# Kernel tuning notes

Hardware: AMD Instinct MI355X
Metric: run time of the kernel (lower is better)

## Reference

```python
import jax, jax.numpy as jnp
import numpy as np

EMBED_DIM = 1024
N_TOKENS = 8192


def setup_inputs() -> dict:
    key = jax.random.key(0)
    k1, k2, k3 = jax.random.split(key, 3)
    inputs = jax.random.normal(k1, (N_TOKENS, EMBED_DIM), dtype=jnp.float32)
    rotation_params = jax.random.normal(k2, (EMBED_DIM, EMBED_DIM), dtype=jnp.float32)
    entangle_params = jax.random.normal(k3, (EMBED_DIM, EMBED_DIM), dtype=jnp.float32)
    return {"inputs": inputs, "rotation_params": rotation_params, "entangle_params": entangle_params}


def reference(inputs, rotation_params, entangle_params):
    # query/key projections from externally supplied params
    embed_dim = inputs.shape[-1]
    wq = rotation_params.reshape(embed_dim, -1)
    wk = entangle_params.reshape(embed_dim, -1)
    query = inputs @ wq          # [N, d]
    key = inputs @ wk            # [N, d]
    scale = 1.0 / jnp.sqrt(jnp.float32(embed_dim))
    scores = jax.nn.softmax(jnp.einsum('nd,md->nm', query, key) * scale, axis=-1)  # [N, N]
    context = scores @ inputs    # attend over raw inputs (V = inputs)
    return context
```

## Files before the change

kernel.cpp:

```cpp
#include <hip/hip_runtime.h>
#include <hip/hip_bf16.h>


typedef _Float16 f16x8 __attribute__((ext_vector_type(8)));
typedef _Float16 f16x4 __attribute__((ext_vector_type(4)));
typedef float    f32x4 __attribute__((ext_vector_type(4)));

#define TM 128
#define TN 128

__device__ __forceinline__ void g2lds16(const _Float16* g, _Float16* l) {
    __builtin_amdgcn_global_load_lds(
        (__attribute__((address_space(1))) unsigned int*)(g),
        (__attribute__((address_space(3))) unsigned int*)(l),
        16, 0, 0);
}


__global__ void prep_x(const float* __restrict__ src,
                       _Float16* __restrict__ hi, _Float16* __restrict__ lo,
                       _Float16* __restrict__ xt, int R, int C) {
    __shared__ float tile[32][33];
    int c0 = blockIdx.x * 32, r0 = blockIdx.y * 32;
    int tx = threadIdx.x, ty = threadIdx.y;
#pragma unroll
    for (int k = 0; k < 4; ++k) {
        int r = ty + 8 * k;
        size_t idx = (size_t)(r0 + r) * C + c0 + tx;
        float v = src[idx];
        tile[r][tx] = v;
        _Float16 h = (_Float16)v;
        hi[idx] = h;
        lo[idx] = (_Float16)(v - (float)h);
    }
    __syncthreads();
#pragma unroll
    for (int k = 0; k < 4; ++k) {
        float v = tile[tx][ty + 8 * k];
        xt[(size_t)(c0 + ty + 8 * k) * R + r0 + tx] = (_Float16)v;
    }
}

__global__ void transpose_split(const float* __restrict__ src,
                                _Float16* __restrict__ dhi,
                                _Float16* __restrict__ dlo,
                                int R, int C) {
    __shared__ float tile[32][33];
    int c0 = blockIdx.x * 32, r0 = blockIdx.y * 32;
    int tx = threadIdx.x, ty = threadIdx.y;
#pragma unroll
    for (int k = 0; k < 4; ++k)
        tile[ty + 8 * k][tx] = src[(size_t)(r0 + ty + 8 * k) * C + c0 + tx];
    __syncthreads();
#pragma unroll
    for (int k = 0; k < 4; ++k) {
        float v = tile[tx][ty + 8 * k];
        _Float16 h = (_Float16)v;
        size_t idx = (size_t)(c0 + ty + 8 * k) * R + r0 + tx;
        dhi[idx] = h;
        dlo[idx] = (_Float16)(v - (float)h);
    }
}

__global__ __launch_bounds__(256) void add_rows(const float* __restrict__ a,
                                                const float* __restrict__ b,
                                                float* __restrict__ out, long n4) {
    long i = (long)blockIdx.x * blockDim.x + threadIdx.x;
    long stride = (long)gridDim.x * blockDim.x;
    for (; i < n4; i += stride) {
        float4 x = ((const float4*)a)[i];
        float4 y = ((const float4*)b)[i];
        x.x += y.x; x.y += y.y; x.z += y.z; x.w += y.w;
        ((float4*)out)[i] = x;
    }
}

template <int TERMS, int SPLIT_OUT, int SWAP, int BKH>
__global__ __launch_bounds__(256, 4) void gemm_bt(
    const _Float16* __restrict__ Ahi, const _Float16* __restrict__ Alo,
    const _Float16* __restrict__ Bhi, const _Float16* __restrict__ Blo,
    float* __restrict__ C, _Float16* __restrict__ Chi, _Float16* __restrict__ Clo,
    long lda, long ldb, long ldc, int K, long zA, long zB, long zC) {
    constexpr int NBUF = (TERMS == 3) ? 4 : 2;
    __shared__ __align__(16) _Float16 s[NBUF * 128 * BKH];

    const long z = blockIdx.z;
    Ahi += z * zA;
    Bhi += z * zB;
    if constexpr (TERMS == 3) { Alo += z * zA; Blo += z * zB; }
    if constexpr (SPLIT_OUT) { Chi += z * zC; Clo += z * zC; }
    else C += z * zC;

    const int t = threadIdx.x;
    const int wave = t >> 6;
    const int lane = t & 63;
    const int lm = lane & 15;
    const int lq = lane >> 4;
    const int wr = wave >> 1;
    const int wc = wave & 1;

    const long rowBase = (long)(SWAP ? blockIdx.x : blockIdx.y) * TM;
    const long colBase = (long)(SWAP ? blockIdx.y : blockIdx.x) * TN;

    const _Float16* src;
    long myLd, gRow0;
    int ldsBaseH;
    if constexpr (TERMS == 3) {
        const _Float16* a = (wave & 1) ? Alo : Ahi;
        const _Float16* b = (wave & 1) ? Blo : Bhi;
        src = (wave & 2) ? b : a;
        myLd = (wave & 2) ? ldb : lda;
        gRow0 = (wave & 2) ? colBase : rowBase;
        ldsBaseH = wave * (128 * BKH);
    } else {
        src = (wave & 2) ? Bhi : Ahi;
        myLd = (wave & 2) ? ldb : lda;
        gRow0 = ((wave & 2) ? colBase : rowBase) + (wave & 1) * 64;
        ldsBaseH = (wave >> 1) * (128 * BKH) + (wave & 1) * (64 * BKH);
    }
    constexpr int LPR = BKH / 8;
    constexpr int RPI = 64 / LPR;
    constexpr int NISS = (TERMS == 3 ? 128 : 64) / RPI;
    const int lr = lane / LPR;
    const int slot = lane % LPR;
    const int swzW = (BKH == 32) ? ((lr >> 1) & 3) : (lr & 7);
    const _Float16* rp = src + (gRow0 + lr) * myLd + (slot ^ swzW) * 8;
    _Float16* ldsW = &s[ldsBaseH];

    const _Float16* sAh = s;
    const _Float16* sBh = s + (TERMS == 3 ? 2 : 1) * 128 * BKH;
    const _Float16* sAl = s + 128 * BKH;
    const _Float16* sBl = s + 3 * 128 * BKH;

    const int swzR = (BKH == 32) ? ((lm >> 1) & 3) : (lm & 7);

    f32x4 acc[4][4];
#pragma unroll
    for (int r = 0; r < 4; ++r)
#pragma unroll
        for (int c = 0; c < 4; ++c)
#pragma unroll
            for (int i = 0; i < 4; ++i) acc[r][c][i] = 0.0f;

    for (int k0 = 0; k0 < K; k0 += BKH) {
        __syncthreads();
#pragma unroll
        for (int j = 0; j < NISS; ++j)
            g2lds16(rp + (long)(j * RPI) * myLd + k0, ldsW + j * 512);
        __syncthreads();

#pragma unroll
        for (int kk = 0; kk < BKH; kk += 32) {
            const int gb = kk >> 3;
            f16x8 ah[4], bh[4], al[4], bl[4];
#pragma unroll
            for (int r = 0; r < 4; ++r) {
                int ra = (wr * 64 + r * 16 + lm) * BKH + ((gb + lq) ^ swzR) * 8;
                int rb = (wc * 64 + r * 16 + lm) * BKH + ((gb + lq) ^ swzR) * 8;
                ah[r] = *(const f16x8*)&sAh[ra];
                bh[r] = *(const f16x8*)&sBh[rb];
                if constexpr (TERMS == 3) {
                    al[r] = *(const f16x8*)&sAl[ra];
                    bl[r] = *(const f16x8*)&sBl[rb];
                }
            }
#pragma unroll
            for (int r = 0; r < 4; ++r)
#pragma unroll
                for (int c = 0; c < 4; ++c) {
                    acc[r][c] = __builtin_amdgcn_mfma_f32_16x16x32_f16(
                        ah[r], bh[c], acc[r][c], 0, 0, 0);
                    if constexpr (TERMS == 3) {
                        acc[r][c] = __builtin_amdgcn_mfma_f32_16x16x32_f16(
                            ah[r], bl[c], acc[r][c], 0, 0, 0);
                        acc[r][c] = __builtin_amdgcn_mfma_f32_16x16x32_f16(
                            al[r], bh[c], acc[r][c], 0, 0, 0);
                    }
                }
        }
    }

#pragma unroll
    for (int r = 0; r < 4; ++r)
#pragma unroll
        for (int c = 0; c < 4; ++c)
#pragma unroll
            for (int i = 0; i < 4; ++i) {
                long row = rowBase + wr * 64 + r * 16 + lq * 4 + i;
                long col = colBase + wc * 64 + c * 16 + lm;
                if constexpr (SPLIT_OUT) {
                    float v = acc[r][c][i];
                    _Float16 h = (_Float16)v;
                    Chi[row * ldc + col] = h;
                    Clo[row * ldc + col] = (_Float16)(v - (float)h);
                } else {
                    C[row * ldc + col] = acc[r][c][i];
                }
            }
}

__global__ __launch_bounds__(256) void softmax_rows(const float* __restrict__ S,
                                                    _Float16* __restrict__ P,
                                                    long ldp, int N) {
    const int row = blockIdx.x;
    const int t = threadIdx.x;
    const float4* rowp = (const float4*)(S + (size_t)row * N);
    float4 v[8];
    float mx = -3.4e38f;
#pragma unroll
    for (int g = 0; g < 4; ++g) {
        v[2 * g]     = rowp[2 * t + 512 * g];
        v[2 * g + 1] = rowp[2 * t + 512 * g + 1];
    }
#pragma unroll
    for (int i = 0; i < 8; ++i)
        mx = fmaxf(mx, fmaxf(fmaxf(v[i].x, v[i].y), fmaxf(v[i].z, v[i].w)));
    __shared__ float red[8];
#pragma unroll
    for (int off = 32; off >= 1; off >>= 1) mx = fmaxf(mx, __shfl_xor(mx, off));
    if ((t & 63) == 0) red[t >> 6] = mx;
    __syncthreads();
    mx = fmaxf(fmaxf(red[0], red[1]), fmaxf(red[2], red[3]));

    float sum = 0.0f;
#pragma unroll
    for (int i = 0; i < 8; ++i) {
        v[i].x = __expf((v[i].x - mx) * 0.03125f);
        v[i].y = __expf((v[i].y - mx) * 0.03125f);
        v[i].z = __expf((v[i].z - mx) * 0.03125f);
        v[i].w = __expf((v[i].w - mx) * 0.03125f);
        sum += (v[i].x + v[i].y) + (v[i].z + v[i].w);
    }
#pragma unroll
    for (int off = 32; off >= 1; off >>= 1) sum += __shfl_xor(sum, off);
    if ((t & 63) == 0) red[4 + (t >> 6)] = sum;
    __syncthreads();
    float inv = 1.0f / (red[4] + red[5] + red[6] + red[7]);

    f16x8* prow = (f16x8*)(P + (size_t)row * ldp);
#pragma unroll
    for (int g = 0; g < 4; ++g) {
        float4 a = v[2 * g], b = v[2 * g + 1];
        f16x8 o;
        o[0] = (_Float16)(a.x * inv); o[1] = (_Float16)(a.y * inv);
        o[2] = (_Float16)(a.z * inv); o[3] = (_Float16)(a.w * inv);
        o[4] = (_Float16)(b.x * inv); o[5] = (_Float16)(b.y * inv);
        o[6] = (_Float16)(b.z * inv); o[7] = (_Float16)(b.w * inv);
        prow[t + 256 * g] = o;
    }
}

extern "C" void kernel_launch(void* const* d_in, const int* in_sizes, int n_in,
                              void* d_out, int out_size, void* d_ws, size_t ws_size,
                              hipStream_t stream) {
    const float* X  = (const float*)d_in[0];
    const float* Wq = (const float*)d_in[1];
    const float* Wk = (const float*)d_in[2];
    float* out = (float*)d_out;

    const long Nt = 8192, D = 1024;
    char* ws = (char*)d_ws;
    const size_t MB = 1024ull * 1024ull;

    _Float16* XT  = (_Float16*)(ws + 0);
    _Float16* Qhi = (_Float16*)(ws + 16 * MB);
    _Float16* Qlo = (_Float16*)(ws + 32 * MB);
    _Float16* Khi = (_Float16*)(ws + 48 * MB);
    _Float16* Klo = (_Float16*)(ws + 64 * MB);
    _Float16* Xhi   = (_Float16*)(ws + 80 * MB);
    _Float16* Xlo   = (_Float16*)(ws + 96 * MB);
    _Float16* WqThi = (_Float16*)(ws + 112 * MB);
    _Float16* WqTlo = (_Float16*)(ws + 114 * MB);
    _Float16* WkThi = (_Float16*)(ws + 116 * MB);
    _Float16* WkTlo = (_Float16*)(ws + 118 * MB);
    float* PK0 = (float*)(ws + 16 * MB);

    const size_t rowBytes = (size_t)Nt * 4;
    const bool planA = ws_size >= 208 * MB + 128 * rowBytes;
    _Float16* Pbuf = (_Float16*)(ws + 80 * MB);
    float* Sc;
    long chunk;
    if (planA) {
        Sc = (float*)(ws + 208 * MB);
        size_t avail = ws_size - 208 * MB;
        chunk = (long)((avail / rowBytes / 128) * 128);
    } else {
        Sc = (float*)(ws + 80 * MB);
        size_t avail = ws_size > 80 * MB ? ws_size - 80 * MB : 0;
        chunk = (long)((avail / rowBytes / 128) * 128);
        if (chunk < 128) chunk = 128;
    }
    if (chunk > Nt) chunk = Nt;
    {
        long nch = (Nt + chunk - 1) / chunk;
        chunk = (((Nt + nch - 1) / nch) + 127) / 128 * 128;
    }

    prep_x<<<dim3(32, 256), dim3(32, 8), 0, stream>>>(X, Xhi, Xlo, XT,
                                                      (int)Nt, (int)D);
    transpose_split<<<dim3(32, 32), dim3(32, 8), 0, stream>>>(Wq, WqThi, WqTlo,
                                                              (int)D, (int)D);
    transpose_split<<<dim3(32, 32), dim3(32, 8), 0, stream>>>(Wk, WkThi, WkTlo,
                                                              (int)D, (int)D);

    gemm_bt<3, 1, 1, 32><<<dim3(Nt / TM, D / TN, 2), 256, 0, stream>>>(
        Xhi, Xlo, WqThi, WqTlo, nullptr, Qhi, Qlo, D, D, D, (int)D,
        0, (long)(4 * MB / 2), (long)(32 * MB / 2));

    long done = 0;
    while (done < Nt) {
        long cur = Nt - done < chunk ? Nt - done : chunk;
        gemm_bt<3, 0, 0, 32><<<dim3(Nt / TN, cur / TM, 1), 256, 0, stream>>>(
            Qhi + done * D, Qlo + done * D, Khi, Klo, Sc, nullptr, nullptr,
            D, D, Nt, (int)D, 0, 0, 0);
        if (planA) {
            softmax_rows<<<(int)cur, 256, 0, stream>>>(Sc, Pbuf + done * Nt,
                                                       Nt, (int)Nt);
        } else {
            softmax_rows<<<(int)cur, 256, 0, stream>>>(Sc, (_Float16*)Sc,
                                                       2 * Nt, (int)Nt);
            gemm_bt<1, 0, 1, 64><<<dim3(cur / TM, D / TN, 1), 256, 0, stream>>>(
                (const _Float16*)Sc, nullptr, XT, nullptr,
                out + done * D, nullptr, nullptr, 2 * Nt, Nt, D, (int)Nt,
                0, 0, 0);
        }
        done += cur;
    }

    if (planA) {
        gemm_bt<1, 0, 1, 64><<<dim3(Nt / TM, D / TN, 2), 256, 0, stream>>>(
            Pbuf, nullptr, XT, nullptr, PK0, nullptr, nullptr,
            Nt, Nt, D, (int)(Nt / 2),
            Nt / 2, Nt / 2, Nt * D);
        add_rows<<<1024, 256, 0, stream>>>(PK0, PK0 + Nt * D, out, Nt * D / 4);
    }
}
```

Baseline: 814.4 us.

## Double-buffer score chunks and fuse previous chunk's softmax into next QK GEMM

The score buffer is split into two ping-pong halves. The QK^T GEMM for chunk i now launches extra blocks that run the softmax for chunk i-1, so softmax overlaps GEMM work inside one launch and the separate softmax launches mostly go away. The trade-off is smaller chunks, since each buffer gets half the space, plus heterogeneous blocks in the GEMM grid. Fused softmax blocks share the GEMM kernel's launch bounds and LDS footprint, which could affect occupancy.

```diff
diff --git a/kernel.cpp b/kernel.cpp
--- a/kernel.cpp
+++ b/kernel.cpp
@@ -75,12 +75,76 @@
     }
 }
 
-template <int TERMS, int SPLIT_OUT, int SWAP, int BKH>
+__device__ __forceinline__ void softmax_row_body(const float* __restrict__ rowS,
+                                                 _Float16* __restrict__ rowP) {
+    const int t = threadIdx.x;
+    const float4* rowp = (const float4*)rowS;
+    float4 v[8];
+    float mx = -3.4e38f;
+#pragma unroll
+    for (int g = 0; g < 4; ++g) {
+        v[2 * g]     = rowp[2 * t + 512 * g];
+        v[2 * g + 1] = rowp[2 * t + 512 * g + 1];
+    }
+#pragma unroll
+    for (int i = 0; i < 8; ++i)
+        mx = fmaxf(mx, fmaxf(fmaxf(v[i].x, v[i].y), fmaxf(v[i].z, v[i].w)));
+    __shared__ float red[8];
+#pragma unroll
+    for (int off = 32; off >= 1; off >>= 1) mx = fmaxf(mx, __shfl_xor(mx, off));
+    if ((t & 63) == 0) red[t >> 6] = mx;
+    __syncthreads();
+    mx = fmaxf(fmaxf(red[0], red[1]), fmaxf(red[2], red[3]));
+
+    float sum = 0.0f;
+#pragma unroll
+    for (int i = 0; i < 8; ++i) {
+        v[i].x = __expf((v[i].x - mx) * 0.03125f);
+        v[i].y = __expf((v[i].y - mx) * 0.03125f);
+        v[i].z = __expf((v[i].z - mx) * 0.03125f);
+        v[i].w = __expf((v[i].w - mx) * 0.03125f);
+        sum += (v[i].x + v[i].y) + (v[i].z + v[i].w);
+    }
+#pragma unroll
+    for (int off = 32; off >= 1; off >>= 1) sum += __shfl_xor(sum, off);
+    if ((t & 63) == 0) red[4 + (t >> 6)] = sum;
+    __syncthreads();
+    float inv = 1.0f / (red[4] + red[5] + red[6] + red[7]);
+
+    f16x8* prow = (f16x8*)rowP;
+#pragma unroll
+    for (int g = 0; g < 4; ++g) {
+        float4 a = v[2 * g], b = v[2 * g + 1];
+        f16x8 o;
+        o[0] = (_Float16)(a.x * inv); o[1] = (_Float16)(a.y * inv);
+        o[2] = (_Float16)(a.z * inv); o[3] = (_Float16)(a.w * inv);
+        o[4] = (_Float16)(b.x * inv); o[5] = (_Float16)(b.y * inv);
+        o[6] = (_Float16)(b.z * inv); o[7] = (_Float16)(b.w * inv);
+        prow[t + 256 * g] = o;
+    }
+}
+
+__global__ __launch_bounds__(256) void softmax_rows(const float* __restrict__ S,
+                                                    _Float16* __restrict__ P,
+                                                    long ldp, int N) {
+    softmax_row_body(S + (size_t)blockIdx.x * N, P + (size_t)blockIdx.x * ldp);
+}
+
+template <int TERMS, int SPLIT_OUT, int SWAP, int BKH, int FUSE>
 __global__ __launch_bounds__(256, 4) void gemm_bt(
     const _Float16* __restrict__ Ahi, const _Float16* __restrict__ Alo,
     const _Float16* __restrict__ Bhi, const _Float16* __restrict__ Blo,
     float* __restrict__ C, _Float16* __restrict__ Chi, _Float16* __restrict__ Clo,
-    long lda, long ldb, long ldc, int K, long zA, long zB, long zC) {
+    long lda, long ldb, long ldc, int K, long zA, long zB, long zC,
+    const float* __restrict__ smS, _Float16* __restrict__ smP,
+    long smLdp, int smY) {
+    if constexpr (FUSE) {
+        if ((int)blockIdx.y < smY) {
+            long row = (long)blockIdx.y * 64 + blockIdx.x;
+            softmax_row_body(smS + row * 8192, smP + row * smLdp);
+            return;
+        }
+    }
     constexpr int NBUF = (TERMS == 3) ? 4 : 2;
     __shared__ __align__(16) _Float16 s[NBUF * 128 * BKH];
 
@@ -91,6 +155,7 @@
     if constexpr (SPLIT_OUT) { Chi += z * zC; Clo += z * zC; }
     else C += z * zC;
 
+    const int by = (int)blockIdx.y - (FUSE ? smY : 0);
     const int t = threadIdx.x;
     const int wave = t >> 6;
     const int lane = t & 63;
@@ -99,8 +164,8 @@
     const int wr = wave >> 1;
     const int wc = wave & 1;
 
-    const long rowBase = (long)(SWAP ? blockIdx.x : blockIdx.y) * TM;
-    const long colBase = (long)(SWAP ? blockIdx.y : blockIdx.x) * TN;
+    const long rowBase = (long)(SWAP ? (int)blockIdx.x : by) * TM;
+    const long colBase = (long)(SWAP ? by : (int)blockIdx.x) * TN;
 
     const _Float16* src;
     long myLd, gRow0;
@@ -199,57 +264,6 @@
             }
 }
 
-__global__ __launch_bounds__(256) void softmax_rows(const float* __restrict__ S,
-                                                    _Float16* __restrict__ P,
-                                                    long ldp, int N) {
-    const int row = blockIdx.x;
-    const int t = threadIdx.x;
-    const float4* rowp = (const float4*)(S + (size_t)row * N);
-    float4 v[8];
-    float mx = -3.4e38f;
-#pragma unroll
-    for (int g = 0; g < 4; ++g) {
-        v[2 * g]     = rowp[2 * t + 512 * g];
-        v[2 * g + 1] = rowp[2 * t + 512 * g + 1];
-    }
-#pragma unroll
-    for (int i = 0; i < 8; ++i)
-        mx = fmaxf(mx, fmaxf(fmaxf(v[i].x, v[i].y), fmaxf(v[i].z, v[i].w)));
-    __shared__ float red[8];
-#pragma unroll
-    for (int off = 32; off >= 1; off >>= 1) mx = fmaxf(mx, __shfl_xor(mx, off));
-    if ((t & 63) == 0) red[t >> 6] = mx;
-    __syncthreads();
-    mx = fmaxf(fmaxf(red[0], red[1]), fmaxf(red[2], red[3]));
-
-    float sum = 0.0f;
-#pragma unroll
-    for (int i = 0; i < 8; ++i) {
-        v[i].x = __expf((v[i].x - mx) * 0.03125f);
-        v[i].y = __expf((v[i].y - mx) * 0.03125f);
-        v[i].z = __expf((v[i].z - mx) * 0.03125f);
-        v[i].w = __expf((v[i].w - mx) * 0.03125f);
-        sum += (v[i].x + v[i].y) + (v[i].z + v[i].w);
-    }
-#pragma unroll
-    for (int off = 32; off >= 1; off >>= 1) sum += __shfl_xor(sum, off);
-    if ((t & 63) == 0) red[4 + (t >> 6)] = sum;
-    __syncthreads();
-    float inv = 1.0f / (red[4] + red[5] + red[6] + red[7]);
-
-    f16x8* prow = (f16x8*)(P + (size_t)row * ldp);
-#pragma unroll
-    for (int g = 0; g < 4; ++g) {
-        float4 a = v[2 * g], b = v[2 * g + 1];
-        f16x8 o;
-        o[0] = (_Float16)(a.x * inv); o[1] = (_Float16)(a.y * inv);
-        o[2] = (_Float16)(a.z * inv); o[3] = (_Float16)(a.w * inv);
-        o[4] = (_Float16)(b.x * inv); o[5] = (_Float16)(b.y * inv);
-        o[6] = (_Float16)(b.z * inv); o[7] = (_Float16)(b.w * inv);
-        prow[t + 256 * g] = o;
-    }
-}
-
 extern "C" void kernel_launch(void* const* d_in, const int* in_sizes, int n_in,
                               void* d_out, int out_size, void* d_ws, size_t ws_size,
                               hipStream_t stream) {
@@ -278,23 +292,6 @@
     const size_t rowBytes = (size_t)Nt * 4;
     const bool planA = ws_size >= 208 * MB + 128 * rowBytes;
     _Float16* Pbuf = (_Float16*)(ws + 80 * MB);
-    float* Sc;
-    long chunk;
-    if (planA) {
-        Sc = (float*)(ws + 208 * MB);
-        size_t avail = ws_size - 208 * MB;
-        chunk = (long)((avail / rowBytes / 128) * 128);
-    } else {
-        Sc = (float*)(ws + 80 * MB);
-        size_t avail = ws_size > 80 * MB ? ws_size - 80 * MB : 0;
-        chunk = (long)((avail / rowBytes / 128) * 128);
-        if (chunk < 128) chunk = 128;
-    }
-    if (chunk > Nt) chunk = Nt;
-    {
-        long nch = (Nt + chunk - 1) / chunk;
-        chunk = (((Nt + nch - 1) / nch) + 127) / 128 * 128;
-    }
 
     prep_x<<<dim3(32, 256), dim3(32, 8), 0, stream>>>(X, Xhi, Xlo, XT,
                                                       (int)Nt, (int)D);
@@ -303,35 +300,90 @@
     transpose_split<<<dim3(32, 32), dim3(32, 8), 0, stream>>>(Wk, WkThi, WkTlo,
                                                               (int)D, (int)D);
 
-    gemm_bt<3, 1, 1, 32><<<dim3(Nt / TM, D / TN, 2), 256, 0, stream>>>(
+    gemm_bt<3, 1, 1, 32, 0><<<dim3(Nt / TM, D / TN, 2), 256, 0, stream>>>(
         Xhi, Xlo, WqThi, WqTlo, nullptr, Qhi, Qlo, D, D, D, (int)D,
-        0, (long)(4 * MB / 2), (long)(32 * MB / 2));
-
-    long done = 0;
-    while (done < Nt) {
-        long cur = Nt - done < chunk ? Nt - done : chunk;
-        gemm_bt<3, 0, 0, 32><<<dim3(Nt / TN, cur / TM, 1), 256, 0, stream>>>(
-            Qhi + done * D, Qlo + done * D, Khi, Klo, Sc, nullptr, nullptr,
-            D, D, Nt, (int)D, 0, 0, 0);
-        if (planA) {
-            softmax_rows<<<(int)cur, 256, 0, stream>>>(Sc, Pbuf + done * Nt,
-                                                       Nt, (int)Nt);
+        0, (long)(4 * MB / 2), (long)(32 * MB / 2),
+        nullptr, nullptr, 0, 0);
+
+    if (planA) {
+        size_t avail = ws_size - 208 * MB;
+        long maxC = (long)((avail / 2 / rowBytes / 128) * 128);
+        const bool pp = maxC >= 128;
+        long chunk;
+        if (pp) {
+            if (maxC > Nt) maxC = Nt;
+            long nch = (Nt + maxC - 1) / maxC;
+            chunk = (((Nt + nch - 1) / nch) + 127) / 128 * 128;
         } else {
+            chunk = (long)((avail / rowBytes / 128) * 128);
+            if (chunk > Nt) chunk = Nt;
+            long nch = (Nt + chunk - 1) / chunk;
+            chunk = (((Nt + nch - 1) / nch) + 127) / 128 * 128;
+        }
+        float* Sc0 = (float*)(ws + 208 * MB);
+        float* Sc1 = pp ? (float*)(ws + 208 * MB + (size_t)chunk * rowBytes)
+                        : Sc0;
+
+        long done = 0, prevDone = 0, prevCur = 0;
+        int i = 0;
+        while (done < Nt) {
+            long cur = Nt - done < chunk ? Nt - done : chunk;
+            float* Scur = (i & 1) ? Sc1 : Sc0;
+            if (pp) {
+                float* Sprev = (i & 1) ? Sc0 : Sc1;
+                int smY = (int)(prevCur / 64);
+                gemm_bt<3, 0, 0, 32, 1>
+                    <<<dim3(Nt / TN, smY + cur / TM, 1), 256, 0, stream>>>(
+                    Qhi + done * D, Qlo + done * D, Khi, Klo, Scur,
+                    nullptr, nullptr, D, D, Nt, (int)D, 0, 0, 0,
+                    Sprev, Pbuf + prevDone * Nt, Nt, smY);
+            } else {
+                gemm_bt<3, 0, 0, 32, 0>
+                    <<<dim3(Nt / TN, cur / TM, 1), 256, 0, stream>>>(
+                    Qhi + done * D, Qlo + done * D, Khi, Klo, Scur,
+                    nullptr, nullptr, D, D, Nt, (int)D, 0, 0, 0,
+                    nullptr, nullptr, 0, 0);
+                softmax_rows<<<(int)cur, 256, 0, stream>>>(
+                    Scur, Pbuf + done * Nt, Nt, (int)Nt);
+            }
+            prevDone = done; prevCur = cur;
+            done += cur; ++i;
+        }
+        if (pp) {
+            float* Sprev = (i & 1) ? Sc0 : Sc1;
+            softmax_rows<<<(int)prevCur, 256, 0, stream>>>(
+                Sprev, Pbuf + prevDone * Nt, Nt, (int)Nt);
+        }
+
+        gemm_bt<1, 0, 1, 64, 0><<<dim3(Nt / TM, D / TN, 2), 256, 0, stream>>>(
+            Pbuf, nullptr, XT, nullptr, PK0, nullptr, nullptr,
+            Nt, Nt, D, (int)(Nt / 2),
+            Nt / 2, Nt / 2, Nt * D,
+            nullptr, nullptr, 0, 0);
+        add_rows<<<1024, 256, 0, stream>>>(PK0, PK0 + Nt * D, out, Nt * D / 4);
+    } else {
+        float* Sc = (float*)(ws + 80 * MB);
+        size_t avail = ws_size > 80 * MB ? ws_size - 80 * MB : 0;
+        long chunk = (long)((avail / rowBytes / 128) * 128);
+        if (chunk < 128) chunk = 128;
+        if (chunk > Nt) chunk = Nt;
+        long nch = (Nt + chunk - 1) / chunk;
+        chunk = (((Nt + nch - 1) / nch) + 127) / 128 * 128;
+        long done = 0;
+        while (done < Nt) {
+            long cur = Nt - done < chunk ? Nt - done : chunk;
+            gemm_bt<3, 0, 0, 32, 0>
+                <<<dim3(Nt / TN, cur / TM, 1), 256, 0, stream>>>(
+                Qhi + done * D, Qlo + done * D, Khi, Klo, Sc, nullptr, nullptr,
+                D, D, Nt, (int)D, 0, 0, 0, nullptr, nullptr, 0, 0);
             softmax_rows<<<(int)cur, 256, 0, stream>>>(Sc, (_Float16*)Sc,
                                                        2 * Nt, (int)Nt);
-            gemm_bt<1, 0, 1, 64><<<dim3(cur / TM, D / TN, 1), 256, 0, stream>>>(
+            gemm_bt<1, 0, 1, 64, 0>
+                <<<dim3(cur / TM, D / TN, 1), 256, 0, stream>>>(
                 (const _Float16*)Sc, nullptr, XT, nullptr,
                 out + done * D, nullptr, nullptr, 2 * Nt, Nt, D, (int)Nt,
-                0, 0, 0);
-        }
-        done += cur;
-    }
-
-    if (planA) {
-        gemm_bt<1, 0, 1, 64><<<dim3(Nt / TM, D / TN, 2), 256, 0, stream>>>(
-            Pbuf, nullptr, XT, nullptr, PK0, nullptr, nullptr,
-            Nt, Nt, D, (int)(Nt / 2),
-            Nt / 2, Nt / 2, Nt * D);
-        add_rows<<<1024, 256, 0, stream>>>(PK0, PK0 + Nt * D, out, Nt * D / 4);
-    }
-}
+                0, 0, 0, nullptr, nullptr, 0, 0);
+            done += cur;
+        }
+    }
+}
```

New measurement: 878.7 us. 7.9% more time.

## Fuse chunked score GEMM with previous chunk's PV GEMM in one launch

Applied to the files above, without the earlier changes.

In the large-workspace plan, each chunk's QK^T score GEMM now runs in the same launch as the P·V GEMM of the previous chunk. Blocks are split by blockIdx.y, so the two independent workloads fill the GPU together. This replaces the old final split-K PV GEMM and the add_rows reduction, removing the fp32 partial buffers and their extra memory traffic. The two Wq/Wk transposes are also merged into one launch. It relies on a software-pipelined chunk schedule and uses a fixed shared-memory size for both GEMM variants, which may reduce occupancy for the smaller-tile variant.

```diff
diff --git a/kernel.cpp b/kernel.cpp
--- a/kernel.cpp
+++ b/kernel.cpp
@@ -3,7 +3,6 @@
 
 
 typedef _Float16 f16x8 __attribute__((ext_vector_type(8)));
-typedef _Float16 f16x4 __attribute__((ext_vector_type(4)));
 typedef float    f32x4 __attribute__((ext_vector_type(4)));
 
 #define TM 128
@@ -41,11 +40,15 @@
     }
 }
 
-__global__ void transpose_split(const float* __restrict__ src,
-                                _Float16* __restrict__ dhi,
-                                _Float16* __restrict__ dlo,
-                                int R, int C) {
+__global__ void transpose_split2(const float* __restrict__ srcQ,
+                                 const float* __restrict__ srcK,
+                                 _Float16* __restrict__ dhi,
+                                 _Float16* __restrict__ dlo,
+                                 int R, int C, long zOff) {
     __shared__ float tile[32][33];
+    const float* src = blockIdx.z ? srcK : srcQ;
+    _Float16* hi = dhi + blockIdx.z * zOff;
+    _Float16* lo = dlo + blockIdx.z * zOff;
     int c0 = blockIdx.x * 32, r0 = blockIdx.y * 32;
     int tx = threadIdx.x, ty = threadIdx.y;
 #pragma unroll
@@ -57,40 +60,19 @@
         float v = tile[tx][ty + 8 * k];
         _Float16 h = (_Float16)v;
         size_t idx = (size_t)(c0 + ty + 8 * k) * R + r0 + tx;
-        dhi[idx] = h;
-        dlo[idx] = (_Float16)(v - (float)h);
-    }
-}
-
-__global__ __launch_bounds__(256) void add_rows(const float* __restrict__ a,
-                                                const float* __restrict__ b,
-                                                float* __restrict__ out, long n4) {
-    long i = (long)blockIdx.x * blockDim.x + threadIdx.x;
-    long stride = (long)gridDim.x * blockDim.x;
-    for (; i < n4; i += stride) {
-        float4 x = ((const float4*)a)[i];
-        float4 y = ((const float4*)b)[i];
-        x.x += y.x; x.y += y.y; x.z += y.z; x.w += y.w;
-        ((float4*)out)[i] = x;
-    }
-}
-
-template <int TERMS, int SPLIT_OUT, int SWAP, int BKH>
-__global__ __launch_bounds__(256, 4) void gemm_bt(
+        hi[idx] = h;
+        lo[idx] = (_Float16)(v - (float)h);
+    }
+}
+
+template <int TERMS, int SPLIT_OUT, int BKH>
+__device__ __forceinline__ void gemm_core(
     const _Float16* __restrict__ Ahi, const _Float16* __restrict__ Alo,
     const _Float16* __restrict__ Bhi, const _Float16* __restrict__ Blo,
-    float* __restrict__ C, _Float16* __restrict__ Chi, _Float16* __restrict__ Clo,
-    long lda, long ldb, long ldc, int K, long zA, long zB, long zC) {
-    constexpr int NBUF = (TERMS == 3) ? 4 : 2;
-    __shared__ __align__(16) _Float16 s[NBUF * 128 * BKH];
-
-    const long z = blockIdx.z;
-    Ahi += z * zA;
-    Bhi += z * zB;
-    if constexpr (TERMS == 3) { Alo += z * zA; Blo += z * zB; }
-    if constexpr (SPLIT_OUT) { Chi += z * zC; Clo += z * zC; }
-    else C += z * zC;
-
+    float* __restrict__ C, _Float16* __restrict__ Chi,
+    _Float16* __restrict__ Clo,
+    long lda, long ldb, long ldc, int K,
+    long rowBase, long colBase, _Float16* s) {
     const int t = threadIdx.x;
     const int wave = t >> 6;
     const int lane = t & 63;
@@ -98,9 +80,6 @@
     const int lq = lane >> 4;
     const int wr = wave >> 1;
     const int wc = wave & 1;
-
-    const long rowBase = (long)(SWAP ? blockIdx.x : blockIdx.y) * TM;
-    const long colBase = (long)(SWAP ? blockIdx.y : blockIdx.x) * TN;
 
     const _Float16* src;
     long myLd, gRow0;
@@ -199,6 +178,47 @@
             }
 }
 
+template <int TERMS, int SPLIT_OUT, int SWAP, int BKH>
+__global__ __launch_bounds__(256, 4) void gemm_bt(
+    const _Float16* __restrict__ Ahi, const _Float16* __restrict__ Alo,
+    const _Float16* __restrict__ Bhi, const _Float16* __restrict__ Blo,
+    float* __restrict__ C, _Float16* __restrict__ Chi, _Float16* __restrict__ Clo,
+    long lda, long ldb, long ldc, int K, long zA, long zB, long zC) {
+    __shared__ __align__(16) _Float16 s[16384];
+    const long z = blockIdx.z;
+    Ahi += z * zA;
+    Bhi += z * zB;
+    if constexpr (TERMS == 3) { Alo += z * zA; Blo += z * zB; }
+    if constexpr (SPLIT_OUT) { Chi += z * zC; Clo += z * zC; }
+    else C += z * zC;
+    const long rowBase = (long)(SWAP ? blockIdx.x : blockIdx.y) * TM;
+    const long colBase = (long)(SWAP ? blockIdx.y : blockIdx.x) * TN;
+    gemm_core<TERMS, SPLIT_OUT, BKH>(Ahi, Alo, Bhi, Blo, C, Chi, Clo,
+                                     lda, ldb, ldc, K, rowBase, colBase, s);
+}
+
+__global__ __launch_bounds__(256, 4) void sgemm_pv(
+    const _Float16* __restrict__ Qh, const _Float16* __restrict__ Ql,
+    const _Float16* __restrict__ Kh, const _Float16* __restrict__ Kl,
+    float* __restrict__ Sc, int gemmY,
+    const _Float16* __restrict__ P, const _Float16* __restrict__ XT,
+    float* __restrict__ Out, int pvNB) {
+    __shared__ __align__(16) _Float16 s[16384];
+    const long Nt = 8192, D = 1024;
+    if ((int)blockIdx.y < gemmY) {
+        gemm_core<3, 0, 32>(Qh, Ql, Kh, Kl, Sc, nullptr, nullptr,
+                            D, D, Nt, (int)D,
+                            (long)blockIdx.y * TM, (long)blockIdx.x * TN, s);
+    } else {
+        int idx = ((int)blockIdx.y - gemmY) * 64 + (int)blockIdx.x;
+        if (idx >= pvNB) return;
+        int rb = idx >> 3, cb = idx & 7;
+        gemm_core<1, 0, 64>(P, nullptr, XT, nullptr, Out, nullptr, nullptr,
+                            Nt, Nt, D, (int)Nt,
+                            (long)rb * TM, (long)cb * TN, s);
+    }
+}
+
 __global__ __launch_bounds__(256) void softmax_rows(const float* __restrict__ S,
                                                     _Float16* __restrict__ P,
                                                     long ldp, int N) {
@@ -271,67 +291,73 @@
     _Float16* Xlo   = (_Float16*)(ws + 96 * MB);
     _Float16* WqThi = (_Float16*)(ws + 112 * MB);
     _Float16* WqTlo = (_Float16*)(ws + 114 * MB);
-    _Float16* WkThi = (_Float16*)(ws + 116 * MB);
-    _Float16* WkTlo = (_Float16*)(ws + 118 * MB);
-    float* PK0 = (float*)(ws + 16 * MB);
 
     const size_t rowBytes = (size_t)Nt * 4;
     const bool planA = ws_size >= 208 * MB + 128 * rowBytes;
     _Float16* Pbuf = (_Float16*)(ws + 80 * MB);
-    float* Sc;
-    long chunk;
-    if (planA) {
-        Sc = (float*)(ws + 208 * MB);
-        size_t avail = ws_size - 208 * MB;
-        chunk = (long)((avail / rowBytes / 128) * 128);
-    } else {
-        Sc = (float*)(ws + 80 * MB);
-        size_t avail = ws_size > 80 * MB ? ws_size - 80 * MB : 0;
-        chunk = (long)((avail / rowBytes / 128) * 128);
-        if (chunk < 128) chunk = 128;
-    }
-    if (chunk > Nt) chunk = Nt;
-    {
-        long nch = (Nt + chunk - 1) / chunk;
-        chunk = (((Nt + nch - 1) / nch) + 127) / 128 * 128;
-    }
 
     prep_x<<<dim3(32, 256), dim3(32, 8), 0, stream>>>(X, Xhi, Xlo, XT,
                                                       (int)Nt, (int)D);
-    transpose_split<<<dim3(32, 32), dim3(32, 8), 0, stream>>>(Wq, WqThi, WqTlo,
-                                                              (int)D, (int)D);
-    transpose_split<<<dim3(32, 32), dim3(32, 8), 0, stream>>>(Wk, WkThi, WkTlo,
-                                                              (int)D, (int)D);
+    transpose_split2<<<dim3(32, 32, 2), dim3(32, 8), 0, stream>>>(
+        Wq, Wk, WqThi, WqTlo, (int)D, (int)D, (long)(4 * MB / 2));
 
     gemm_bt<3, 1, 1, 32><<<dim3(Nt / TM, D / TN, 2), 256, 0, stream>>>(
         Xhi, Xlo, WqThi, WqTlo, nullptr, Qhi, Qlo, D, D, D, (int)D,
         0, (long)(4 * MB / 2), (long)(32 * MB / 2));
 
-    long done = 0;
-    while (done < Nt) {
-        long cur = Nt - done < chunk ? Nt - done : chunk;
-        gemm_bt<3, 0, 0, 32><<<dim3(Nt / TN, cur / TM, 1), 256, 0, stream>>>(
-            Qhi + done * D, Qlo + done * D, Khi, Klo, Sc, nullptr, nullptr,
-            D, D, Nt, (int)D, 0, 0, 0);
-        if (planA) {
-            softmax_rows<<<(int)cur, 256, 0, stream>>>(Sc, Pbuf + done * Nt,
-                                                       Nt, (int)Nt);
-        } else {
+    if (planA) {
+        float* Sc = (float*)(ws + 208 * MB);
+        size_t avail = ws_size - 208 * MB;
+        long chunk = (long)((avail / rowBytes / 128) * 128);
+        if (chunk > Nt) chunk = Nt;
+        long nch = (Nt + chunk - 1) / chunk;
+        chunk = (((Nt + nch - 1) / nch) + 127) / 128 * 128;
+
+        long done = 0, prevDone = 0, prevCur = 0;
+        int c = 0;
+        while (done < Nt) {
+            long cur = Nt - done < chunk ? Nt - done : chunk;
+            int gemmY = (int)(cur / TM);
+            int pvNB = (c >= 1) ? (int)(prevCur / TM) * 8 : 0;
+            int pvY = (pvNB + 63) / 64;
+            sgemm_pv<<<dim3(Nt / TN, gemmY + pvY), 256, 0, stream>>>(
+                Qhi + done * D, Qlo + done * D, Khi, Klo, Sc, gemmY,
+                Pbuf + prevDone * Nt, XT, out + prevDone * D, pvNB);
+            softmax_rows<<<(int)cur, 256, 0, stream>>>(
+                Sc, Pbuf + done * Nt, Nt, (int)Nt);
+            prevDone = done; prevCur = cur;
+            done += cur; ++c;
+        }
+        {
+            int pvNB = (int)(prevCur / TM) * 8;
+            int pvY = (pvNB + 63) / 64;
+            sgemm_pv<<<dim3(Nt / TN, pvY), 256, 0, stream>>>(
+                Qhi, Qlo, Khi, Klo, Sc, 0,
+                Pbuf + prevDone * Nt, XT, out + prevDone * D, pvNB);
+        }
+    } else {
+        float* Sc = (float*)(ws + 80 * MB);
+        size_t avail = ws_size > 80 * MB ? ws_size - 80 * MB : 0;
+        long chunk = (long)((avail / rowBytes / 128) * 128);
+        if (chunk < 128) chunk = 128;
+        if (chunk > Nt) chunk = Nt;
+        long nch = (Nt + chunk - 1) / chunk;
+        chunk = (((Nt + nch - 1) / nch) + 127) / 128 * 128;
+        long done = 0;
+        while (done < Nt) {
+            long cur = Nt - done < chunk ? Nt - done : chunk;
+            gemm_bt<3, 0, 0, 32>
+                <<<dim3(Nt / TN, cur / TM, 1), 256, 0, stream>>>(
+                Qhi + done * D, Qlo + done * D, Khi, Klo, Sc, nullptr, nullptr,
+                D, D, Nt, (int)D, 0, 0, 0);
             softmax_rows<<<(int)cur, 256, 0, stream>>>(Sc, (_Float16*)Sc,
                                                        2 * Nt, (int)Nt);
-            gemm_bt<1, 0, 1, 64><<<dim3(cur / TM, D / TN, 1), 256, 0, stream>>>(
+            gemm_bt<1, 0, 1, 64>
+                <<<dim3(cur / TM, D / TN, 1), 256, 0, stream>>>(
                 (const _Float16*)Sc, nullptr, XT, nullptr,
                 out + done * D, nullptr, nullptr, 2 * Nt, Nt, D, (int)Nt,
                 0, 0, 0);
+            done += cur;
         }
-        done += cur;
-    }
-
-    if (planA) {
-        gemm_bt<1, 0, 1, 64><<<dim3(Nt / TM, D / TN, 2), 256, 0, stream>>>(
-            Pbuf, nullptr, XT, nullptr, PK0, nullptr, nullptr,
-            Nt, Nt, D, (int)(Nt / 2),
-            Nt / 2, Nt / 2, Nt * D);
-        add_rows<<<1024, 256, 0, stream>>>(PK0, PK0 + Nt * D, out, Nt * D / 4);
-    }
-}
+    }
+}
```

Result: slower. 1.245 ms (+52.9%).
